# Kernel optimization log

Hardware: AMD Instinct MI355X
Metric: run time of the kernel (lower is better)

## Reference

```python
import jax, jax.numpy as jnp
import numpy as np

B, S, D, H, FF = 4, 1024, 1024, 8, 4096
DK = D // H
EPS = 1e-5


def layernorm(x, g, b):
    m = jnp.mean(x, axis=-1, keepdims=True)
    v = jnp.mean(jnp.square(x - m), axis=-1, keepdims=True)
    return (x - m) * jax.lax.rsqrt(v + EPS) * g + b


def setup_inputs() -> dict:
    key = jax.random.key(0)
    ks = jax.random.split(key, 8)
    w = lambda k, shape: jax.random.normal(k, shape, jnp.float32) * 0.02
    return {
        "x": jax.random.normal(ks[0], (B, S, D), jnp.float32),
        "mask": jnp.ones((B, 1, 1, S), jnp.int32),  # unused in 'infer' mode, kept for fidelity
        "g1": jnp.ones((D,), jnp.float32), "b1": jnp.zeros((D,), jnp.float32),
        "Wq": w(ks[1], (D, D)), "bq": jnp.zeros((D,), jnp.float32),
        "Wk": w(ks[2], (D, D)), "bk": jnp.zeros((D,), jnp.float32),
        "Wv": w(ks[3], (D, H * D)), "bv": jnp.zeros((H * D,), jnp.float32),
        "g2": jnp.ones((D,), jnp.float32), "b2": jnp.zeros((D,), jnp.float32),
        "W1": w(ks[4], (D, FF)), "bw1": jnp.zeros((FF,), jnp.float32),
        "W2": w(ks[5], (FF, D)), "bw2": jnp.zeros((D,), jnp.float32),
    }


def reference(x, mask, g1, b1, Wq, bq, Wk, bk, Wv, bv, g2, b2, W1, bw1, W2, bw2):
    # --- MultiHeadedAttention (mode='infer'; mask is ignored by this path) ---
    xn = layernorm(x, g1, b1)                                   # [B,S,D]
    q = (xn @ Wq + bq).reshape(B, S, H, DK).transpose(0, 2, 1, 3)  # [B,H,S,DK]
    k = (xn @ Wk + bk).reshape(B, S, H, DK).transpose(0, 2, 1, 3)  # [B,H,S,DK]
    v = (xn @ Wv + bv).reshape(B, S, H, D).transpose(0, 2, 1, 3)   # [B,H,S,D]
    scores = jnp.einsum('bhqd,bhkd->bhqk', q, k) / jnp.sqrt(jnp.float32(DK))
    p = jax.nn.softmax(scores, axis=-1)                          # [B,H,S,S]
    ctx = jnp.einsum('bhqk,bhkd->bhqd', p, v)                    # [B,H,S,D]
    # Source does x.view(-1, B, dim, h).sum(heads).view(B, S, dim) on the
    # contiguous [B,H,S,D] tensor: a raw row-major reshape, reproduced exactly.
    attn_out = ctx.reshape(S, B, D, H).sum(axis=-1).reshape(B, S, D)
    # --- residual + SublayerConnection (pre-norm GELU FFN) ---
    x1 = x + attn_out
    xn2 = layernorm(x1, g2, b2)
    ffn = jax.nn.gelu(xn2 @ W1 + bw1, approximate=False) @ W2 + bw2
    return x1 + ffn
```

## Files before the change

### kernel.cpp

```cpp
#include <hip/hip_runtime.h>
#include <hip/hip_bf16.h>
#include <math.h>

typedef __attribute__((ext_vector_type(8))) short   short8;
typedef __attribute__((ext_vector_type(4))) short   short4v;
typedef __attribute__((ext_vector_type(8))) __bf16  bf16x8;
typedef __attribute__((ext_vector_type(4))) float   f32x4;

typedef const __attribute__((address_space(1))) void cgv_t;
typedef __attribute__((address_space(3))) void lv_t;

__device__ __forceinline__ float bs2f(short s) {
  unsigned int u = ((unsigned int)(unsigned short)s) << 16;
  return __builtin_bit_cast(float, u);
}
__device__ __forceinline__ short f2bs(float f) {
  __hip_bfloat16 h = __float2bfloat16(f);
  return __builtin_bit_cast(short, h);
}
__device__ __forceinline__ void glds16(const short* g, short* l) {
  __builtin_amdgcn_global_load_lds((cgv_t*)g, (lv_t*)l, 16, 0, 0);
}


__global__ __launch_bounds__(256) void transpose_k(const float* __restrict__ in,
                                                   short* __restrict__ out,
                                                   int R, int C) {
  __shared__ __align__(16) short T[64 * 72];
  const int r0 = blockIdx.y * 64, c0 = blockIdx.x * 64;
  const int t = threadIdx.x;
  {
    const int rr = t >> 4;
    const int cc = (t & 15) << 2;
#pragma unroll
    for (int h = 0; h < 4; h++) {
      const int row = rr + h * 16;
      f32x4 v = *(const f32x4*)(in + (long)(r0 + row) * C + c0 + cc);
#pragma unroll
      for (int e = 0; e < 4; e++) T[row * 72 + cc + e] = f2bs(v[e]);
    }
  }
  __syncthreads();
  {
    const int cr = t >> 3;
    const int rs = (t & 7) << 3;
#pragma unroll
    for (int h = 0; h < 2; h++) {
      const int c = cr + h * 32;
      short8 v;
#pragma unroll
      for (int e = 0; e < 8; e++) v[e] = T[(rs + e) * 72 + c];
      *(short8*)(out + (long)(c0 + c) * R + r0 + rs) = v;
    }
  }
}

__global__ __launch_bounds__(256) void wv8_k(const float* __restrict__ Wv,
                                             short* __restrict__ out) {
  __shared__ __align__(16) short T[64 * 72];
  const int r0 = blockIdx.x * 64, k0 = blockIdx.y * 64;
  const int t = threadIdx.x;
  const int wave = t >> 6, lane = t & 63;
  const int r = r0 + lane;
#pragma unroll 4
  for (int i = 0; i < 16; i++) {
    const int k = k0 + wave * 16 + i;
    const float* src = Wv + (long)k * 8192 + 8 * r;
    f32x4 a = *(const f32x4*)src;
    f32x4 b = *(const f32x4*)(src + 4);
    float s = (a[0] + a[1] + a[2] + a[3]) + (b[0] + b[1] + b[2] + b[3]);
    T[lane * 72 + wave * 16 + i] = f2bs(s);
  }
  __syncthreads();
  const int rr = t >> 3, kc = (t & 7) << 3;
#pragma unroll
  for (int half = 0; half < 2; half++) {
    const int rl = rr + half * 32;
    *(short8*)(out + (long)(r0 + rl) * 1024 + k0 + kc) = *(const short8*)&T[rl * 72 + kc];
  }
}

__global__ __launch_bounds__(256) void bv8_k(const float* __restrict__ bv,
                                             float* __restrict__ out) {
  const int r = blockIdx.x * 256 + threadIdx.x;
  f32x4 a = *(const f32x4*)(bv + 8 * r);
  f32x4 b = *(const f32x4*)(bv + 8 * r + 4);
  out[r] = (a[0] + a[1] + a[2] + a[3]) + (b[0] + b[1] + b[2] + b[3]);
}

__global__ __launch_bounds__(256) void ln_k(const float* __restrict__ in,
                                            const float* __restrict__ g,
                                            const float* __restrict__ b,
                                            short* __restrict__ out) {
  const int t = threadIdx.x;
  const long base = (long)blockIdx.x * 1024 + t * 4;
  f32x4 f = *(const f32x4*)(in + base);
  float v[4] = {f[0], f[1], f[2], f[3]};
  float s1 = v[0] + v[1] + v[2] + v[3];
  float s2 = v[0]*v[0] + v[1]*v[1] + v[2]*v[2] + v[3]*v[3];
#pragma unroll
  for (int off = 32; off; off >>= 1) {
    s1 += __shfl_xor(s1, off);
    s2 += __shfl_xor(s2, off);
  }
  __shared__ float rs[4], rq[4];
  if ((t & 63) == 0) { rs[t >> 6] = s1; rq[t >> 6] = s2; }
  __syncthreads();
  s1 = rs[0] + rs[1] + rs[2] + rs[3];
  s2 = rq[0] + rq[1] + rq[2] + rq[3];
  const float mean = s1 * (1.0f / 1024.0f);
  const float var  = s2 * (1.0f / 1024.0f) - mean * mean;
  const float rstd = rsqrtf(var + 1e-5f);
  f32x4 gv = *(const f32x4*)(g + t * 4);
  f32x4 bv = *(const f32x4*)(b + t * 4);
  short4v o;
#pragma unroll
  for (int i = 0; i < 4; i++)
    o[i] = f2bs((v[i] - mean) * rstd * gv[i] + bv[i]);
  *(short4v*)(out + base) = o;
}

__global__ __launch_bounds__(256) void reduce2_k(const float* __restrict__ p0,
                                                 const float* __restrict__ p1,
                                                 const float* __restrict__ x1,
                                                 const float* __restrict__ bias,
                                                 float* __restrict__ out) {
  const int t = threadIdx.x;
  const long base = (long)blockIdx.x * 1024 + t * 4;
  f32x4 a = *(const f32x4*)(p0 + base);
  f32x4 b = *(const f32x4*)(p1 + base);
  f32x4 c = *(const f32x4*)(x1 + base);
  f32x4 d = *(const f32x4*)(bias + t * 4);
  *(f32x4*)(out + base) = a + b + c + d;
}

__global__ __launch_bounds__(256, 2) void flash_k(
    const short* __restrict__ Qg_, const short* __restrict__ Kg_,
    const short* __restrict__ V8T, const float* __restrict__ xg,
    float* __restrict__ x1) {
  __shared__ __align__(16) short smem[40960];
  short* Qs = smem;
  short* Ks = smem + 8192;
  short* Vs = smem + 24576;

  const int t = threadIdx.x;
  const int wave = t >> 6, lane = t & 63;
  const int llo = lane & 15, lhi = lane >> 4;
  const int q0 = blockIdx.x * 64;
  const int bh = blockIdx.y, b = bh >> 3, h = bh & 7;
  const float SC = 0.0883883476483184f;

  const short* Qg = Qg_ + ((long)(b * 1024 + q0)) * 1024 + h * 128;
  const short* Kg = Kg_ + ((long)b * 1024) * 1024 + h * 128;
  const short* Vg = V8T + (long)bh * 131072;

  const int srow = t >> 2, schunk = (t & 3) << 3;
  const int wbase = wave * 512;
  const int arow = (wave * 16 + llo) * 32 + lhi * 8;

#pragma unroll
  for (int kk = 0; kk < 4; kk++)
    glds16(Qg + (long)srow * 1024 + kk * 32 + schunk, Qs + kk * 2048 + wbase);

  f32x4 o[8];
  float mR[4], lR[4];
#pragma unroll
  for (int i = 0; i < 8; i++) o[i] = f32x4{0.f, 0.f, 0.f, 0.f};
#pragma unroll
  for (int r = 0; r < 4; r++) { mR[r] = -1e30f; lR[r] = 0.f; }

  for (int it = 0; it < 8; it++) {
    const int kt0 = it * 128;
#pragma unroll
    for (int kk = 0; kk < 4; kk++) {
      glds16(Kg + (long)(kt0 + srow) * 1024 + kk * 32 + schunk,
             Ks + kk * 4096 + wbase);
      glds16(Kg + (long)(kt0 + 64 + srow) * 1024 + kk * 32 + schunk,
             Ks + kk * 4096 + 2048 + wbase);
      glds16(Vg + (long)srow * 1024 + kt0 + kk * 32 + schunk,
             Vs + kk * 4096 + wbase);
      glds16(Vg + (long)(64 + srow) * 1024 + kt0 + kk * 32 + schunk,
             Vs + kk * 4096 + 2048 + wbase);
    }
    __syncthreads();

    f32x4 s[8];
#pragma unroll
    for (int i = 0; i < 8; i++) s[i] = f32x4{0.f, 0.f, 0.f, 0.f};
#pragma unroll
    for (int kk = 0; kk < 4; kk++) {
      bf16x8 aq = *(const bf16x8*)(Qs + kk * 2048 + arow);
#pragma unroll
      for (int ct = 0; ct < 8; ct++) {
        bf16x8 bk = *(const bf16x8*)(Ks + kk * 4096 + (ct * 16 + llo) * 32 + lhi * 8);
        s[ct] = __builtin_amdgcn_mfma_f32_16x16x32_bf16(aq, bk, s[ct], 0, 0, 0);
      }
    }
#pragma unroll
    for (int ct = 0; ct < 8; ct++)
#pragma unroll
      for (int r = 0; r < 4; r++) s[ct][r] *= SC;
    float alpha[4];
#pragma unroll
    for (int r = 0; r < 4; r++) {
      float mt = s[0][r];
#pragma unroll
      for (int ct = 1; ct < 8; ct++) mt = fmaxf(mt, s[ct][r]);
      mt = fmaxf(mt, __shfl_xor(mt, 1));
      mt = fmaxf(mt, __shfl_xor(mt, 2));
      mt = fmaxf(mt, __shfl_xor(mt, 4));
      mt = fmaxf(mt, __shfl_xor(mt, 8));
      const float mn = fmaxf(mR[r], mt);
      alpha[r] = expf(mR[r] - mn);
      mR[r] = mn;
    }
#pragma unroll
    for (int ct = 0; ct < 8; ct++)
#pragma unroll
      for (int r = 0; r < 4; r++) s[ct][r] = expf(s[ct][r] - mR[r]);
#pragma unroll
    for (int ct = 0; ct < 8; ct++)
#pragma unroll
      for (int r = 0; r < 4; r++) o[ct][r] *= alpha[r];
#pragma unroll
    for (int r = 0; r < 4; r++) {
      float ls = s[0][r];
#pragma unroll
      for (int ct = 1; ct < 8; ct++) ls += s[ct][r];
      ls += __shfl_xor(ls, 1);
      ls += __shfl_xor(ls, 2);
      ls += __shfl_xor(ls, 4);
      ls += __shfl_xor(ls, 8);
      lR[r] = lR[r] * alpha[r] + ls;
    }
    __syncthreads();

#pragma unroll
    for (int ct = 0; ct < 8; ct++) {
      const int base = (ct >> 1) * 4096 + ((ct & 1) << 4) + llo;
#pragma unroll
      for (int r = 0; r < 4; r++)
        Ks[base + (wave * 16 + lhi * 4 + r) * 32] = f2bs(s[ct][r]);
    }
    __syncthreads();

#pragma unroll
    for (int kk = 0; kk < 4; kk++) {
      bf16x8 ap = *(const bf16x8*)(Ks + kk * 4096 + arow);
#pragma unroll
      for (int ct = 0; ct < 8; ct++) {
        bf16x8 bv = *(const bf16x8*)(Vs + kk * 4096 + (ct * 16 + llo) * 32 + lhi * 8);
        o[ct] = __builtin_amdgcn_mfma_f32_16x16x32_bf16(ap, bv, o[ct], 0, 0, 0);
      }
    }
    __syncthreads();
  }

  float inv[4];
#pragma unroll
  for (int r = 0; r < 4; r++) inv[r] = 1.0f / lR[r];
#pragma unroll
  for (int ct = 0; ct < 8; ct++) {
#pragma unroll
    for (int r = 0; r < 4; r++) {
      const int row = q0 + wave * 16 + lhi * 4 + r;
      const long idx = ((long)(b * 8 + h) * 1024 + row) * 128 + ct * 16 + llo;
      x1[idx] = xg[idx] + o[ct][r] * inv[r];
    }
  }
}

enum { EPI_GELU = 4, EPI_QKV8 = 6, EPI_PART = 8 };

template <int EPI, int BN, int NS>
__global__ __launch_bounds__(256) void gemm128(
    const short* __restrict__ A, int lda, long azh, long azl,
    const short* __restrict__ Bt, int ldb, long bzh, long bzl,
    const float* __restrict__ bias, long biasl,
    void* __restrict__ outp, long czl, int ldc,
    const void* __restrict__ aux,
    int K) {
  constexpr int WH = (BN == 128) ? 64 : 32;
  constexpr int RT = WH / 16;
  constexpr int ASLAB = 4096;
  constexpr int BSLAB = BN * 32;
  constexpr int STAGE = NS * (ASLAB + BSLAB);
  constexpr int SMEM_SHORTS = (EPI == EPI_QKV8 && STAGE < 17408) ? 17408 : STAGE;
  __shared__ __align__(16) short smem[SMEM_SHORTS];
  short* As = smem;
  short* Bs = smem + NS * ASLAB;

  const int t = threadIdx.x;
  const int wave = t >> 6, lane = t & 63;
  const int llo = lane & 15, lhi = lane >> 4;
  const int wm = (BN == 128) ? (wave >> 1) : wave;
  const int wn = (BN == 128) ? (wave & 1) : 0;
  const int bn0 = blockIdx.x * BN, bm0 = blockIdx.y * 128;
  const int z = blockIdx.z;
  const int zh = z >> 3, zl = z & 7;

  const short* Ab = A + (long)zh * azh + (long)zl * azl;
  const short* Bb = Bt + (long)zh * bzh + (long)zl * bzl;
  bias += (long)zl * biasl;

  f32x4 acc[RT][4];
#pragma unroll
  for (int i = 0; i < RT; i++)
#pragma unroll
    for (int j = 0; j < 4; j++) acc[i][j] = f32x4{0.f, 0.f, 0.f, 0.f};

  const int srow = t >> 2, schunk = (t & 3) << 3;
  const short* Ag0 = Ab + (long)(bm0 + srow) * lda + schunk;
  const short* Ag1 = Ab + (long)(bm0 + 64 + srow) * lda + schunk;
  const short* Bg0 = Bb + (long)(bn0 + srow) * ldb + schunk;
  const short* Bg1 = Bb + (long)(bn0 + 64 + srow) * ldb + schunk;
  short* AsW0 = As + (wave * 16) * 32;
  short* AsW1 = As + (64 + wave * 16) * 32;
  short* BsW0 = Bs + (wave * 16) * 32;
  short* BsW1 = Bs + (64 + wave * 16) * 32;

  const short* aRd = As + (wm * WH + llo) * 32 + lhi * 8;
  const short* bRd = Bs + (wn * 64 + llo) * 32 + lhi * 8;

  for (int kt = 0; kt < K; kt += 32 * NS) {
#pragma unroll
    for (int s = 0; s < NS; s++) {
      glds16(Ag0 + kt + s * 32, AsW0 + s * ASLAB);
      glds16(Ag1 + kt + s * 32, AsW1 + s * ASLAB);
      glds16(Bg0 + kt + s * 32, BsW0 + s * BSLAB);
      if (BN == 128) glds16(Bg1 + kt + s * 32, BsW1 + s * BSLAB);
    }
    __syncthreads();
#pragma unroll
    for (int s = 0; s < NS; s++) {
      bf16x8 af[RT], bf[4];
#pragma unroll
      for (int i = 0; i < RT; i++)
        af[i] = *(const bf16x8*)(aRd + s * ASLAB + i * 16 * 32);
#pragma unroll
      for (int j = 0; j < 4; j++)
        bf[j] = *(const bf16x8*)(bRd + s * BSLAB + j * 16 * 32);
#pragma unroll
      for (int rt = 0; rt < RT; rt++)
#pragma unroll
        for (int ct = 0; ct < 4; ct++)
          acc[rt][ct] = __builtin_amdgcn_mfma_f32_16x16x32_bf16(af[rt], bf[ct], acc[rt][ct], 0, 0, 0);
    }
    __syncthreads();
  }

  if (EPI == EPI_GELU || (EPI == EPI_QKV8 && blockIdx.z < 2)) {
    short* C = (short*)outp + (long)z * czl;
#pragma unroll
    for (int ct = 0; ct < 4; ct++) {
      const int col = bn0 + wn * 64 + ct * 16 + llo;
      const float bval = bias[col];
#pragma unroll
      for (int rt = 0; rt < RT; rt++) {
#pragma unroll
        for (int r = 0; r < 4; r++) {
          const int row = bm0 + wm * WH + rt * 16 + lhi * 4 + r;
          float v = acc[rt][ct][r] + bval;
          if (EPI == EPI_GELU) v = 0.5f * v * (1.0f + erff(v * 0.70710678118654752f));
          C[(long)row * ldc + col] = f2bs(v);
        }
      }
    }
  } else if (EPI == EPI_QKV8) {
    short* Ts = smem;
#pragma unroll
    for (int ct = 0; ct < 4; ct++) {
      const int c = wn * 64 + ct * 16 + llo;
      const float bval = bias[bn0 + c];
#pragma unroll
      for (int rt = 0; rt < RT; rt++) {
#pragma unroll
        for (int r = 0; r < 4; r++) {
          const int row = wm * WH + rt * 16 + lhi * 4 + r;
          Ts[c * 136 + row] = f2bs(acc[rt][ct][r] + bval);
        }
      }
    }
    __syncthreads();
    const int bb = bm0 >> 10, s0 = bm0 & 1023, head = bn0 >> 7;
    short* dstbase = (short*)aux + ((long)(bb * 8 + head)) * 131072 + s0;
    const int sc8 = (t & 15) << 3;
    const int cb = t >> 4;
#pragma unroll
    for (int j = 0; j < 8; j++) {
      const int c = cb + j * 16;
      *(short8*)(dstbase + (long)c * 1024 + sc8) = *(const short8*)&Ts[c * 136 + sc8];
    }
  } else if (EPI == EPI_PART) {
    float* C = (float*)outp + (long)z * czl;
#pragma unroll
    for (int ct = 0; ct < 4; ct++) {
      const int col = bn0 + wn * 64 + ct * 16 + llo;
#pragma unroll
      for (int rt = 0; rt < RT; rt++) {
#pragma unroll
        for (int r = 0; r < 4; r++) {
          const int row = bm0 + wm * WH + rt * 16 + lhi * 4 + r;
          C[(long)row * ldc + col] = acc[rt][ct][r];
        }
      }
    }
  }
}

#define MF16(va, vb, vc) __builtin_amdgcn_mfma_f32_16x16x32_bf16(va, vb, vc, 0, 0, 0)
#define VMW(n) asm volatile("s_waitcnt vmcnt(" #n ")" ::: "memory")
#define NOPS ((void)0)

#define STAGE_A(BUF, KH, KB) do {                                          \
    glds16(Ag + (KB), smem + ((BUF) * 2 + (KH)) * 8192 + wofs);            \
    glds16(Ag2 + (KB), smem + ((BUF) * 2 + (KH)) * 8192 + 4096 + wofs);    \
  } while (0)
#define STAGE_B(BUF, KH, KB) do {                                          \
    glds16(Bg + (KB), smem + 32768 + ((BUF) * 2 + (KH)) * 8192 + wofs);    \
    glds16(Bg2 + (KB), smem + 32768 + ((BUF) * 2 + (KH)) * 8192 + 4096 + wofs); \
  } while (0)

#define PHASE(RH, KH, BUF, LOADB, STAGE_STMT, WAIT_STMT)                   \
  {                                                                        \
    const short* Ar_ = smem + ((BUF) * 2 + (KH)) * 8192 + aoff + (RH) * 2048; \
    bf16x8 a0 = *(const bf16x8*)(Ar_);                                     \
    bf16x8 a1 = *(const bf16x8*)(Ar_ + 512);                               \
    bf16x8 a2 = *(const bf16x8*)(Ar_ + 1024);                              \
    bf16x8 a3 = *(const bf16x8*)(Ar_ + 1536);                              \
    if (LOADB) {                                                           \
      const short* Br_ = smem + 32768 + ((BUF) * 2 + (KH)) * 8192 + boff;  \
      vb0 = *(const bf16x8*)(Br_);                                         \
      vb1 = *(const bf16x8*)(Br_ + 512);                                   \
      vb2 = *(const bf16x8*)(Br_ + 1024);                                  \
      vb3 = *(const bf16x8*)(Br_ + 1536);                                  \
    }                                                                      \
    STAGE_STMT;                                                            \
    __builtin_amdgcn_sched_barrier(0);                                     \
    __builtin_amdgcn_s_barrier();                                          \
    asm volatile("s_waitcnt lgkmcnt(0)" ::: "memory");                     \
    __builtin_amdgcn_sched_barrier(0);                                     \
    __builtin_amdgcn_s_setprio(1);                                         \
    acc[(RH) * 4 + 0][0] = MF16(a0, vb0, acc[(RH) * 4 + 0][0]);            \
    acc[(RH) * 4 + 0][1] = MF16(a0, vb1, acc[(RH) * 4 + 0][1]);            \
    acc[(RH) * 4 + 0][2] = MF16(a0, vb2, acc[(RH) * 4 + 0][2]);            \
    acc[(RH) * 4 + 0][3] = MF16(a0, vb3, acc[(RH) * 4 + 0][3]);            \
    acc[(RH) * 4 + 1][0] = MF16(a1, vb0, acc[(RH) * 4 + 1][0]);            \
    acc[(RH) * 4 + 1][1] = MF16(a1, vb1, acc[(RH) * 4 + 1][1]);            \
    acc[(RH) * 4 + 1][2] = MF16(a1, vb2, acc[(RH) * 4 + 1][2]);            \
    acc[(RH) * 4 + 1][3] = MF16(a1, vb3, acc[(RH) * 4 + 1][3]);            \
    acc[(RH) * 4 + 2][0] = MF16(a2, vb0, acc[(RH) * 4 + 2][0]);            \
    acc[(RH) * 4 + 2][1] = MF16(a2, vb1, acc[(RH) * 4 + 2][1]);            \
    acc[(RH) * 4 + 2][2] = MF16(a2, vb2, acc[(RH) * 4 + 2][2]);            \
    acc[(RH) * 4 + 2][3] = MF16(a2, vb3, acc[(RH) * 4 + 2][3]);            \
    acc[(RH) * 4 + 3][0] = MF16(a3, vb0, acc[(RH) * 4 + 3][0]);            \
    acc[(RH) * 4 + 3][1] = MF16(a3, vb1, acc[(RH) * 4 + 3][1]);            \
    acc[(RH) * 4 + 3][2] = MF16(a3, vb2, acc[(RH) * 4 + 3][2]);            \
    acc[(RH) * 4 + 3][3] = MF16(a3, vb3, acc[(RH) * 4 + 3][3]);            \
    __builtin_amdgcn_s_setprio(0);                                         \
    WAIT_STMT;                                                             \
    __builtin_amdgcn_sched_barrier(0);                                     \
    __builtin_amdgcn_s_barrier();                                          \
  }

#define TILE8(T, BUF)                                                        \
  PHASE(0, 0, BUF, 1, STAGE_A(1 - (BUF), 1, ((T) + 1) * 64 + 32), NOPS);     \
  PHASE(1, 0, BUF, 0, STAGE_B(1 - (BUF), 1, ((T) + 1) * 64 + 32), VMW(8));   \
  PHASE(0, 1, BUF, 1, STAGE_A(BUF, 0, ((T) + 2) * 64), NOPS);                \
  PHASE(1, 1, BUF, 0, STAGE_B(BUF, 0, ((T) + 2) * 64), VMW(8))

__global__ __launch_bounds__(512, 2) void gemm256_gelu(
    const short* __restrict__ A, int lda,
    const short* __restrict__ Bt, int ldb,
    const float* __restrict__ bias,
    short* __restrict__ C, int ldc, int K) {
  __shared__ __align__(16) short smem[65536];

  const int t = threadIdx.x;
  const int wave = t >> 6, lane = t & 63;
  const int llo = lane & 15, lhi = lane >> 4;
  const int wm = wave >> 2, wn = wave & 3;
  const int bm0 = blockIdx.y * 256, bn0 = blockIdx.x * 256;

  const int srow = t >> 2;
  const int sgc = (((t & 3) ^ ((t >> 3) & 3)) << 3);
  const short* Ag  = A  + (long)(bm0 + srow) * lda + sgc;
  const short* Ag2 = A  + (long)(bm0 + 128 + srow) * lda + sgc;
  const short* Bg  = Bt + (long)(bn0 + srow) * ldb + sgc;
  const short* Bg2 = Bt + (long)(bn0 + 128 + srow) * ldb + sgc;
  const int wofs = wave * 512;

  const int swz = ((lhi ^ ((llo >> 1) & 3)) << 3);
  const int aoff = (wm * 128 + llo) * 32 + swz;
  const int boff = (wn * 64 + llo) * 32 + swz;

  f32x4 acc[8][4];
#pragma unroll
  for (int i = 0; i < 8; i++)
#pragma unroll
    for (int j = 0; j < 4; j++) acc[i][j] = f32x4{0.f, 0.f, 0.f, 0.f};
  bf16x8 vb0, vb1, vb2, vb3;

  const int NT = K >> 6;

  STAGE_A(0, 0, 0);  STAGE_B(0, 0, 0);
  STAGE_A(0, 1, 32); STAGE_B(0, 1, 32);
  STAGE_A(1, 0, 64); STAGE_B(1, 0, 64);
  VMW(8);
  __builtin_amdgcn_s_barrier();

  for (int tt = 0; tt < NT - 2; tt += 2) {
    TILE8(tt, 0);
    TILE8(tt + 1, 1);
  }
  PHASE(0, 0, 0, 1, STAGE_A(1, 1, (NT - 1) * 64 + 32), NOPS);
  PHASE(1, 0, 0, 0, STAGE_B(1, 1, (NT - 1) * 64 + 32), VMW(8));
  PHASE(0, 1, 0, 1, NOPS, NOPS);
  PHASE(1, 1, 0, 0, NOPS, VMW(4));
  PHASE(0, 0, 1, 1, NOPS, NOPS);
  PHASE(1, 0, 1, 0, NOPS, VMW(0));
  PHASE(0, 1, 1, 1, NOPS, NOPS);
  PHASE(1, 1, 1, 0, NOPS, NOPS);

  short* slab = smem + wave * 4864;
  float bv4[4];
#pragma unroll
  for (int ct = 0; ct < 4; ct++) bv4[ct] = bias[bn0 + wn * 64 + ct * 16 + llo];
  const int rl0 = lane >> 3, cb8 = (lane & 7) << 3;
  const short* srd = slab + rl0 * 76 + cb8;
  short* Cw = C + (long)(bm0 + wm * 128 + rl0) * ldc + bn0 + wn * 64 + cb8;
#pragma unroll
  for (int p = 0; p < 2; p++) {
#pragma unroll
    for (int rt4 = 0; rt4 < 4; rt4++) {
#pragma unroll
      for (int ct = 0; ct < 4; ct++) {
#pragma unroll
        for (int r = 0; r < 4; r++) {
          float v = acc[p * 4 + rt4][ct][r] + bv4[ct];
          v = 0.5f * v * (1.0f + erff(v * 0.70710678118654752f));
          slab[(rt4 * 16 + lhi * 4 + r) * 76 + ct * 16 + llo] = f2bs(v);
        }
      }
    }
#pragma unroll
    for (int j = 0; j < 8; j++) {
      short8 v = *(const short8*)(srd + j * 8 * 76);
      *(short8*)(Cw + ((long)p * 64 + j * 8) * ldc) = v;
    }
  }
}

extern "C" void kernel_launch(void* const* d_in, const int* in_sizes, int n_in,
                              void* d_out, int out_size, void* d_ws, size_t ws_size,
                              hipStream_t stream) {
  const float* x   = (const float*)d_in[0];
  const float* g1  = (const float*)d_in[2];
  const float* b1  = (const float*)d_in[3];
  const float* Wq  = (const float*)d_in[4];
  const float* bq  = (const float*)d_in[5];
  const float* Wk  = (const float*)d_in[6];
  const float* bk  = (const float*)d_in[7];
  const float* Wv  = (const float*)d_in[8];
  const float* bv  = (const float*)d_in[9];
  const float* g2  = (const float*)d_in[10];
  const float* b2  = (const float*)d_in[11];
  const float* W1  = (const float*)d_in[12];
  const float* bw1 = (const float*)d_in[13];
  const float* W2  = (const float*)d_in[14];
  const float* bw2 = (const float*)d_in[15];

  char* ws = (char*)d_ws;
  const long MB = 1024 * 1024;
  float* bQKV = (float*)(ws);
  float* x1   = (float*)(ws + 1 * MB);
  short* wqT  = (short*)(ws + 17 * MB);
  short* wkT  = (short*)(ws + 19 * MB);
  short* wv8T = (short*)(ws + 21 * MB);
  short* xn   = (short*)(ws + 23 * MB);
  short* Q    = (short*)(ws + 31 * MB);
  short* Kb   = (short*)(ws + 39 * MB);
  short* V8T  = (short*)(ws + 47 * MB);
  short* xn2  = (short*)(ws + 17 * MB);
  short* Hb   = (short*)(ws + 25 * MB);
  short* w1T  = (short*)(ws + 57 * MB);
  short* w2T  = (short*)(ws + 65 * MB);
  float* part = (float*)(ws + 73 * MB);

  hipMemcpyAsync(bQKV, bq, 4096, hipMemcpyDeviceToDevice, stream);
  hipMemcpyAsync(bQKV + 1024, bk, 4096, hipMemcpyDeviceToDevice, stream);
  bv8_k<<<4, 256, 0, stream>>>(bv, bQKV + 2048);

  transpose_k<<<dim3(16, 16), 256, 0, stream>>>(Wq, wqT, 1024, 1024);
  transpose_k<<<dim3(16, 16), 256, 0, stream>>>(Wk, wkT, 1024, 1024);
  wv8_k<<<dim3(16, 16), 256, 0, stream>>>(Wv, wv8T);

  ln_k<<<4096, 256, 0, stream>>>(x, g1, b1, xn);

  gemm128<EPI_QKV8, 128, 2><<<dim3(8, 32, 3), 256, 0, stream>>>(
      xn, 1024, 0, 0, wqT, 1024, 0, 1048576, bQKV, 1024,
      Q, 4194304, 1024, V8T, 1024);

  flash_k<<<dim3(16, 32), 256, 0, stream>>>(Q, Kb, V8T, x, x1);

  transpose_k<<<dim3(64, 16), 256, 0, stream>>>(W1, w1T, 1024, 4096);
  transpose_k<<<dim3(16, 64), 256, 0, stream>>>(W2, w2T, 4096, 1024);

  ln_k<<<4096, 256, 0, stream>>>(x1, g2, b2, xn2);

  gemm256_gelu<<<dim3(16, 16), 512, 0, stream>>>(
      xn2, 1024, w1T, 1024, bw1, Hb, 4096, 1024);

  gemm128<EPI_PART, 64, 2><<<dim3(16, 32, 2), 256, 0, stream>>>(
      Hb, 4096, 0, 2048, w2T, 4096, 0, 2048, nullptr, 0,
      part, 4194304, 1024, nullptr, 2048);

  reduce2_k<<<4096, 256, 0, stream>>>(part, part + 4194304, x1, bw2,
                                      (float*)d_out);
}
```

Before: 398.6 us.

## Route QKV and FFN2 GEMMs through 256-tile pipelined kernel with split-K and swizzle

Generalizes the 256x256 pipelined GELU GEMM into a templated kernel with GELU, QKV and split-K partial epilogues, and removes the older 128-tile GEMM. The QKV projection now uses the large-tile kernel, writes V row-major to a temp buffer, and a new transpose kernel reorders it into the per-head transposed layout that flash attention expects. The FFN down-projection uses 4-way split-K with the large tile, and the final reduce now sums four partials. A workgroup index remap spreads blocks across XCDs. The extra V transpose pass and the doubled partial-sum traffic are the added costs.

```diff
diff --git a/kernel.cpp b/kernel.cpp
--- a/kernel.cpp
+++ b/kernel.cpp
@@ -52,6 +52,34 @@
       for (int e = 0; e < 8; e++) v[e] = T[(rs + e) * 72 + c];
       *(short8*)(out + (long)(c0 + c) * R + r0 + rs) = v;
     }
+  }
+}
+
+__global__ __launch_bounds__(256) void tr16_k(const short* __restrict__ in,
+                                              short* __restrict__ out) {
+  __shared__ __align__(16) short T[64 * 72];
+  const int c0 = blockIdx.x * 64;
+  const int r0 = blockIdx.y * 64;
+  const int t = threadIdx.x;
+  {
+    const int row = t >> 2, cs = (t & 3) << 4;
+    short8 v0 = *(const short8*)(in + (long)(r0 + row) * 1024 + c0 + cs);
+    short8 v1 = *(const short8*)(in + (long)(r0 + row) * 1024 + c0 + cs + 8);
+    *(short8*)&T[row * 72 + cs] = v0;
+    *(short8*)&T[row * 72 + cs + 8] = v1;
+  }
+  __syncthreads();
+  const int bb = r0 >> 10, s0 = r0 & 1023;
+  const int cr = t >> 3, rs = (t & 7) << 3;
+#pragma unroll
+  for (int half = 0; half < 2; half++) {
+    const int c = cr + half * 32;
+    const int gcol = c0 + c;
+    const int head = gcol >> 7, g = gcol & 127;
+    short8 v;
+#pragma unroll
+    for (int e = 0; e < 8; e++) v[e] = T[(rs + e) * 72 + c];
+    *(short8*)(out + ((long)(bb * 8 + head)) * 131072 + (long)g * 1024 + s0 + rs) = v;
   }
 }
 
@@ -120,18 +148,19 @@
   *(short4v*)(out + base) = o;
 }
 
-__global__ __launch_bounds__(256) void reduce2_k(const float* __restrict__ p0,
-                                                 const float* __restrict__ p1,
+__global__ __launch_bounds__(256) void reduce4_k(const float* __restrict__ p,
                                                  const float* __restrict__ x1,
                                                  const float* __restrict__ bias,
                                                  float* __restrict__ out) {
   const int t = threadIdx.x;
   const long base = (long)blockIdx.x * 1024 + t * 4;
-  f32x4 a = *(const f32x4*)(p0 + base);
-  f32x4 b = *(const f32x4*)(p1 + base);
-  f32x4 c = *(const f32x4*)(x1 + base);
-  f32x4 d = *(const f32x4*)(bias + t * 4);
-  *(f32x4*)(out + base) = a + b + c + d;
+  f32x4 a = *(const f32x4*)(p + base);
+  f32x4 b = *(const f32x4*)(p + 4194304 + base);
+  f32x4 c = *(const f32x4*)(p + 8388608 + base);
+  f32x4 d = *(const f32x4*)(p + 12582912 + base);
+  f32x4 e = *(const f32x4*)(x1 + base);
+  f32x4 g = *(const f32x4*)(bias + t * 4);
+  *(f32x4*)(out + base) = a + b + c + d + e + g;
 }
 
 __global__ __launch_bounds__(256, 2) void flash_k(
@@ -270,143 +299,7 @@
   }
 }
 
-enum { EPI_GELU = 4, EPI_QKV8 = 6, EPI_PART = 8 };
-
-template <int EPI, int BN, int NS>
-__global__ __launch_bounds__(256) void gemm128(
-    const short* __restrict__ A, int lda, long azh, long azl,
-    const short* __restrict__ Bt, int ldb, long bzh, long bzl,
-    const float* __restrict__ bias, long biasl,
-    void* __restrict__ outp, long czl, int ldc,
-    const void* __restrict__ aux,
-    int K) {
-  constexpr int WH = (BN == 128) ? 64 : 32;
-  constexpr int RT = WH / 16;
-  constexpr int ASLAB = 4096;
-  constexpr int BSLAB = BN * 32;
-  constexpr int STAGE = NS * (ASLAB + BSLAB);
-  constexpr int SMEM_SHORTS = (EPI == EPI_QKV8 && STAGE < 17408) ? 17408 : STAGE;
-  __shared__ __align__(16) short smem[SMEM_SHORTS];
-  short* As = smem;
-  short* Bs = smem + NS * ASLAB;
-
-  const int t = threadIdx.x;
-  const int wave = t >> 6, lane = t & 63;
-  const int llo = lane & 15, lhi = lane >> 4;
-  const int wm = (BN == 128) ? (wave >> 1) : wave;
-  const int wn = (BN == 128) ? (wave & 1) : 0;
-  const int bn0 = blockIdx.x * BN, bm0 = blockIdx.y * 128;
-  const int z = blockIdx.z;
-  const int zh = z >> 3, zl = z & 7;
-
-  const short* Ab = A + (long)zh * azh + (long)zl * azl;
-  const short* Bb = Bt + (long)zh * bzh + (long)zl * bzl;
-  bias += (long)zl * biasl;
-
-  f32x4 acc[RT][4];
-#pragma unroll
-  for (int i = 0; i < RT; i++)
-#pragma unroll
-    for (int j = 0; j < 4; j++) acc[i][j] = f32x4{0.f, 0.f, 0.f, 0.f};
-
-  const int srow = t >> 2, schunk = (t & 3) << 3;
-  const short* Ag0 = Ab + (long)(bm0 + srow) * lda + schunk;
-  const short* Ag1 = Ab + (long)(bm0 + 64 + srow) * lda + schunk;
-  const short* Bg0 = Bb + (long)(bn0 + srow) * ldb + schunk;
-  const short* Bg1 = Bb + (long)(bn0 + 64 + srow) * ldb + schunk;
-  short* AsW0 = As + (wave * 16) * 32;
-  short* AsW1 = As + (64 + wave * 16) * 32;
-  short* BsW0 = Bs + (wave * 16) * 32;
-  short* BsW1 = Bs + (64 + wave * 16) * 32;
-
-  const short* aRd = As + (wm * WH + llo) * 32 + lhi * 8;
-  const short* bRd = Bs + (wn * 64 + llo) * 32 + lhi * 8;
-
-  for (int kt = 0; kt < K; kt += 32 * NS) {
-#pragma unroll
-    for (int s = 0; s < NS; s++) {
-      glds16(Ag0 + kt + s * 32, AsW0 + s * ASLAB);
-      glds16(Ag1 + kt + s * 32, AsW1 + s * ASLAB);
-      glds16(Bg0 + kt + s * 32, BsW0 + s * BSLAB);
-      if (BN == 128) glds16(Bg1 + kt + s * 32, BsW1 + s * BSLAB);
-    }
-    __syncthreads();
-#pragma unroll
-    for (int s = 0; s < NS; s++) {
-      bf16x8 af[RT], bf[4];
-#pragma unroll
-      for (int i = 0; i < RT; i++)
-        af[i] = *(const bf16x8*)(aRd + s * ASLAB + i * 16 * 32);
-#pragma unroll
-      for (int j = 0; j < 4; j++)
-        bf[j] = *(const bf16x8*)(bRd + s * BSLAB + j * 16 * 32);
-#pragma unroll
-      for (int rt = 0; rt < RT; rt++)
-#pragma unroll
-        for (int ct = 0; ct < 4; ct++)
-          acc[rt][ct] = __builtin_amdgcn_mfma_f32_16x16x32_bf16(af[rt], bf[ct], acc[rt][ct], 0, 0, 0);
-    }
-    __syncthreads();
-  }
-
-  if (EPI == EPI_GELU || (EPI == EPI_QKV8 && blockIdx.z < 2)) {
-    short* C = (short*)outp + (long)z * czl;
-#pragma unroll
-    for (int ct = 0; ct < 4; ct++) {
-      const int col = bn0 + wn * 64 + ct * 16 + llo;
-      const float bval = bias[col];
-#pragma unroll
-      for (int rt = 0; rt < RT; rt++) {
-#pragma unroll
-        for (int r = 0; r < 4; r++) {
-          const int row = bm0 + wm * WH + rt * 16 + lhi * 4 + r;
-          float v = acc[rt][ct][r] + bval;
-          if (EPI == EPI_GELU) v = 0.5f * v * (1.0f + erff(v * 0.70710678118654752f));
-          C[(long)row * ldc + col] = f2bs(v);
-        }
-      }
-    }
-  } else if (EPI == EPI_QKV8) {
-    short* Ts = smem;
-#pragma unroll
-    for (int ct = 0; ct < 4; ct++) {
-      const int c = wn * 64 + ct * 16 + llo;
-      const float bval = bias[bn0 + c];
-#pragma unroll
-      for (int rt = 0; rt < RT; rt++) {
-#pragma unroll
-        for (int r = 0; r < 4; r++) {
-          const int row = wm * WH + rt * 16 + lhi * 4 + r;
-          Ts[c * 136 + row] = f2bs(acc[rt][ct][r] + bval);
-        }
-      }
-    }
-    __syncthreads();
-    const int bb = bm0 >> 10, s0 = bm0 & 1023, head = bn0 >> 7;
-    short* dstbase = (short*)aux + ((long)(bb * 8 + head)) * 131072 + s0;
-    const int sc8 = (t & 15) << 3;
-    const int cb = t >> 4;
-#pragma unroll
-    for (int j = 0; j < 8; j++) {
-      const int c = cb + j * 16;
-      *(short8*)(dstbase + (long)c * 1024 + sc8) = *(const short8*)&Ts[c * 136 + sc8];
-    }
-  } else if (EPI == EPI_PART) {
-    float* C = (float*)outp + (long)z * czl;
-#pragma unroll
-    for (int ct = 0; ct < 4; ct++) {
-      const int col = bn0 + wn * 64 + ct * 16 + llo;
-#pragma unroll
-      for (int rt = 0; rt < RT; rt++) {
-#pragma unroll
-        for (int r = 0; r < 4; r++) {
-          const int row = bm0 + wm * WH + rt * 16 + lhi * 4 + r;
-          C[(long)row * ldc + col] = acc[rt][ct][r];
-        }
-      }
-    }
-  }
-}
+enum { E_GELU = 0, E_QKV = 1, E_PART = 2 };
 
 #define MF16(va, vb, vc) __builtin_amdgcn_mfma_f32_16x16x32_bf16(va, vb, vc, 0, 0, 0)
 #define VMW(n) asm volatile("s_waitcnt vmcnt(" #n ")" ::: "memory")
@@ -469,18 +362,31 @@
   PHASE(0, 1, BUF, 1, STAGE_A(BUF, 0, ((T) + 2) * 64), NOPS);                \
   PHASE(1, 1, BUF, 0, STAGE_B(BUF, 0, ((T) + 2) * 64), VMW(8))
 
-__global__ __launch_bounds__(512, 2) void gemm256_gelu(
-    const short* __restrict__ A, int lda,
-    const short* __restrict__ Bt, int ldb,
-    const float* __restrict__ bias,
-    short* __restrict__ C, int ldc, int K) {
+template <int EPI>
+__global__ __launch_bounds__(512, 2) void gemm256(
+    const short* __restrict__ A, int lda, long azk,
+    const short* __restrict__ Bt, int ldb, long bzk,
+    const float* __restrict__ bias, long biasl,
+    void* __restrict__ outp, long czl, int ldc,
+    void* __restrict__ aux, int K) {
   __shared__ __align__(16) short smem[65536];
 
   const int t = threadIdx.x;
   const int wave = t >> 6, lane = t & 63;
   const int llo = lane & 15, lhi = lane >> 4;
   const int wm = wave >> 2, wn = wave & 3;
-  const int bm0 = blockIdx.y * 256, bn0 = blockIdx.x * 256;
+
+  int lin = blockIdx.x + gridDim.x * (blockIdx.y + gridDim.y * blockIdx.z);
+  const int nwg = gridDim.x * gridDim.y * gridDim.z;
+  lin = (lin & 7) * (nwg >> 3) + (lin >> 3);
+  const int bx = lin % gridDim.x;
+  const int rem = lin / gridDim.x;
+  const int by = rem % gridDim.y;
+  const int z = rem / gridDim.y;
+
+  const int bm0 = by * 256, bn0 = bx * 256;
+  A += (long)z * azk;
+  Bt += (long)z * bzk;
 
   const int srow = t >> 2;
   const int sgc = (((t & 3) ^ ((t >> 3) & 3)) << 3);
@@ -522,31 +428,51 @@
   PHASE(0, 1, 1, 1, NOPS, NOPS);
   PHASE(1, 1, 1, 0, NOPS, NOPS);
 
-  short* slab = smem + wave * 4864;
-  float bv4[4];
-#pragma unroll
-  for (int ct = 0; ct < 4; ct++) bv4[ct] = bias[bn0 + wn * 64 + ct * 16 + llo];
-  const int rl0 = lane >> 3, cb8 = (lane & 7) << 3;
-  const short* srd = slab + rl0 * 76 + cb8;
-  short* Cw = C + (long)(bm0 + wm * 128 + rl0) * ldc + bn0 + wn * 64 + cb8;
-#pragma unroll
-  for (int p = 0; p < 2; p++) {
-#pragma unroll
-    for (int rt4 = 0; rt4 < 4; rt4++) {
-#pragma unroll
-      for (int ct = 0; ct < 4; ct++) {
+  if (EPI == E_PART) {
+    float* P = (float*)outp + (long)z * czl;
+#pragma unroll
+    for (int ct = 0; ct < 4; ct++) {
+      const int col = bn0 + wn * 64 + ct * 16 + llo;
+#pragma unroll
+      for (int rt = 0; rt < 8; rt++) {
 #pragma unroll
         for (int r = 0; r < 4; r++) {
-          float v = acc[p * 4 + rt4][ct][r] + bv4[ct];
-          v = 0.5f * v * (1.0f + erff(v * 0.70710678118654752f));
-          slab[(rt4 * 16 + lhi * 4 + r) * 76 + ct * 16 + llo] = f2bs(v);
+          const int row = bm0 + wm * 128 + rt * 16 + lhi * 4 + r;
+          P[(long)row * ldc + col] = acc[rt][ct][r];
         }
       }
     }
-#pragma unroll
-    for (int j = 0; j < 8; j++) {
-      short8 v = *(const short8*)(srd + j * 8 * 76);
-      *(short8*)(Cw + ((long)p * 64 + j * 8) * ldc) = v;
+  } else {
+    short* C = (short*)outp + (long)z * czl;
+    if (EPI == E_QKV && z == 2) C = (short*)aux;
+    short* slab = smem + wave * 4864;
+    float bv4[4];
+#pragma unroll
+    for (int ct = 0; ct < 4; ct++)
+      bv4[ct] = bias[z * biasl + bn0 + wn * 64 + ct * 16 + llo];
+    const int rl0 = lane >> 3, cb8 = (lane & 7) << 3;
+    const short* srd = slab + rl0 * 76 + cb8;
+    short* Cw = C + (long)(bm0 + wm * 128 + rl0) * ldc + bn0 + wn * 64 + cb8;
+#pragma unroll
+    for (int p = 0; p < 2; p++) {
+#pragma unroll
+      for (int rt4 = 0; rt4 < 4; rt4++) {
+#pragma unroll
+        for (int ct = 0; ct < 4; ct++) {
+#pragma unroll
+          for (int r = 0; r < 4; r++) {
+            float v = acc[p * 4 + rt4][ct][r] + bv4[ct];
+            if (EPI == E_GELU)
+              v = 0.5f * v * (1.0f + erff(v * 0.70710678118654752f));
+            slab[(rt4 * 16 + lhi * 4 + r) * 76 + ct * 16 + llo] = f2bs(v);
+          }
+        }
+      }
+#pragma unroll
+      for (int j = 0; j < 8; j++) {
+        short8 v = *(const short8*)(srd + j * 8 * 76);
+        *(short8*)(Cw + ((long)p * 64 + j * 8) * ldc) = v;
+      }
     }
   }
 }
@@ -572,15 +498,16 @@
 
   char* ws = (char*)d_ws;
   const long MB = 1024 * 1024;
-  float* bQKV = (float*)(ws);
-  float* x1   = (float*)(ws + 1 * MB);
-  short* wqT  = (short*)(ws + 17 * MB);
-  short* wkT  = (short*)(ws + 19 * MB);
-  short* wv8T = (short*)(ws + 21 * MB);
-  short* xn   = (short*)(ws + 23 * MB);
-  short* Q    = (short*)(ws + 31 * MB);
-  short* Kb   = (short*)(ws + 39 * MB);
-  short* V8T  = (short*)(ws + 47 * MB);
+  float* bQKV  = (float*)(ws);
+  float* x1    = (float*)(ws + 1 * MB);
+  short* wqT   = (short*)(ws + 17 * MB);
+  short* wkT   = (short*)(ws + 19 * MB);
+  short* wv8T  = (short*)(ws + 21 * MB);
+  short* xn    = (short*)(ws + 23 * MB);
+  short* Q     = (short*)(ws + 31 * MB);
+  short* Kb    = (short*)(ws + 39 * MB);
+  short* V8T   = (short*)(ws + 47 * MB);
+  short* V8tmp = (short*)(ws + 55 * MB);
   short* xn2  = (short*)(ws + 17 * MB);
   short* Hb   = (short*)(ws + 25 * MB);
   short* w1T  = (short*)(ws + 57 * MB);
@@ -597,9 +524,11 @@
 
   ln_k<<<4096, 256, 0, stream>>>(x, g1, b1, xn);
 
-  gemm128<EPI_QKV8, 128, 2><<<dim3(8, 32, 3), 256, 0, stream>>>(
-      xn, 1024, 0, 0, wqT, 1024, 0, 1048576, bQKV, 1024,
-      Q, 4194304, 1024, V8T, 1024);
+  gemm256<E_QKV><<<dim3(4, 16, 3), 512, 0, stream>>>(
+      xn, 1024, 0, wqT, 1024, 1048576, bQKV, 1024,
+      Q, 4194304, 1024, V8tmp, 1024);
+
+  tr16_k<<<dim3(16, 64), 256, 0, stream>>>(V8tmp, V8T);
 
   flash_k<<<dim3(16, 32), 256, 0, stream>>>(Q, Kb, V8T, x, x1);
 
@@ -608,13 +537,13 @@
 
   ln_k<<<4096, 256, 0, stream>>>(x1, g2, b2, xn2);
 
-  gemm256_gelu<<<dim3(16, 16), 512, 0, stream>>>(
-      xn2, 1024, w1T, 1024, bw1, Hb, 4096, 1024);
-
-  gemm128<EPI_PART, 64, 2><<<dim3(16, 32, 2), 256, 0, stream>>>(
-      Hb, 4096, 0, 2048, w2T, 4096, 0, 2048, nullptr, 0,
-      part, 4194304, 1024, nullptr, 2048);
-
-  reduce2_k<<<4096, 256, 0, stream>>>(part, part + 4194304, x1, bw2,
-                                      (float*)d_out);
-}
+  gemm256<E_GELU><<<dim3(16, 16, 1), 512, 0, stream>>>(
+      xn2, 1024, 0, w1T, 1024, 0, bw1, 0,
+      Hb, 0, 4096, nullptr, 1024);
+
+  gemm256<E_PART><<<dim3(4, 16, 4), 512, 0, stream>>>(
+      Hb, 4096, 1024, w2T, 4096, 1024, nullptr, 0,
+      part, 4194304, 1024, nullptr, 1024);
+
+  reduce4_k<<<4096, 256, 0, stream>>>(part, x1, bw2, (float*)d_out);
+}
```

Result: faster. 370.2 us (-7.1%).
